# Performance work log

Hardware: AMD Instinct MI355X
Metric: run time of the kernel (lower is better)

The kernel has to match this reference:

```python
import jax, jax.numpy as jnp
import numpy as np

N, E, C, H, L = 20000, 200000, 64, 4, 2
L0_IN, E_IN, L0_OUT = 65, 15, 64
HC = H * C
EPS = 1e-5  # InstanceNorm1d default eps
NEG_SLOPE = 0.01  # F.leaky_relu default used by DGL EGATConv


def setup_inputs() -> dict:
    key = jax.random.key(0)
    ks = jax.random.split(key, 16)
    def s(k, shape, fan):
        return (jax.random.normal(k, shape, jnp.float32) / np.float32(np.sqrt(fan)))
    return {
        "x": jax.random.normal(ks[0], (N, L0_IN), jnp.float32),
        "efeat": jax.random.normal(ks[1], (E, E_IN), jnp.float32),
        "src": jax.random.randint(ks[2], (E,), 0, N, dtype=jnp.int32),
        "dst": jax.random.randint(ks[3], (E,), 0, N, dtype=jnp.int32),
        "Wn0": s(ks[4], (L0_IN, C), L0_IN),
        "bn0": jnp.zeros((C,), jnp.float32),
        "We0": s(ks[5], (E_IN, C), E_IN),
        "be0": jnp.zeros((C,), jnp.float32),
        "Wnode": s(ks[6], (L, C, HC), C),
        "bnode": jnp.zeros((L, HC), jnp.float32),
        "Wni": s(ks[7], (L, C, HC), C),
        "Wnj": s(ks[8], (L, C, HC), C),
        "Wfij": s(ks[9], (L, C, HC), C),
        "attn": s(ks[10], (L, H, C), C),
        "bias_e": jnp.zeros((L, HC), jnp.float32),
        "Wf": s(ks[11], (C, L0_OUT), C),
        "bf": jnp.zeros((L0_OUT,), jnp.float32),
    }


def _inorm(x):
    # InstanceNorm1d on a 2D [rows, channels] tensor == per-row normalization
    m = jnp.mean(x, axis=-1, keepdims=True)
    v = jnp.var(x, axis=-1, keepdims=True)
    return (x - m) * jax.lax.rsqrt(v + EPS)


def reference(x, efeat, src, dst, Wn0, bn0, We0, be0, Wnode, bnode,
              Wni, Wnj, Wfij, attn, bias_e, Wf, bf):
    h = x @ Wn0 + bn0        # [N, C]
    f = efeat @ We0 + be0    # [E, C]
    for l in range(L):
        # edge feature update: f_out = fc_ni(h)[src] + fc_nj(h)[dst] + fc_fij(f) + bias
        f_out = (h @ Wni[l])[src] + (h @ Wnj[l])[dst] + f @ Wfij[l] + bias_e[l]  # [E, HC]
        e = jax.nn.leaky_relu(f_out, NEG_SLOPE).reshape(E, H, C)
        score = jnp.einsum('ehc,hc->eh', e, attn[l])  # [E, H]
        # edge softmax over incoming edges of each destination node
        smax = jax.ops.segment_max(score, dst, num_segments=N)
        w = jnp.exp(score - smax[dst])
        denom = jax.ops.segment_sum(w, dst, num_segments=N)
        a = w / denom[dst]                                # [E, H]
        hproj = (h @ Wnode[l] + bnode[l]).reshape(N, H, C)
        msg = hproj[src] * a[:, :, None]                  # [E, H, C]
        h_new = jax.ops.segment_sum(msg, dst, num_segments=N)  # [N, H, C]
        # mean over heads -> InstanceNorm -> ELU
        h = jax.nn.elu(_inorm(jnp.mean(h_new, axis=1)))
        f = jax.nn.elu(_inorm(jnp.mean(f_out.reshape(E, H, C), axis=1)))
    return h @ Wf + bf
```

## Files before the change

kernel.cpp:

```cpp
#include <hip/hip_runtime.h>
#include <cmath>

#define NN 20000
#define NE 200000
#define SCAN_BLOCKS 79

typedef __attribute__((ext_vector_type(8))) short bf16x8;
typedef __attribute__((ext_vector_type(4))) float f32x4;
typedef unsigned int uint;

__device__ __forceinline__ float4 ld4(const float* p){ return *(const float4*)p; }

__device__ __forceinline__ uint packbf(float a, float b) {
  uint ua = __float_as_uint(a);
  uint ub = __float_as_uint(b);
  ua = (ua + 0x7fffu + ((ua >> 16) & 1u)) >> 16;
  ub = (ub + 0x7fffu + ((ub >> 16) & 1u)) >> 16;
  return ua | (ub << 16);
}
__device__ __forceinline__ float4 up4(uint2 u) {
  return make_float4(__uint_as_float(u.x << 16), __uint_as_float(u.x & 0xffff0000u),
                     __uint_as_float(u.y << 16), __uint_as_float(u.y & 0xffff0000u));
}

__global__ void gemm4_bf16(const float* __restrict__ A, const float* __restrict__ B,
                           const float* __restrict__ bias, uint2* __restrict__ O,
                           int M, int K, int Nout) {
  int jt = Nout >> 2;
  int idx = blockIdx.x * 256 + threadIdx.x;
  if (idx >= M * jt) return;
  int m = idx / jt;
  int j4 = (idx - m * jt) << 2;
  const float* a = A + (long)m * K;
  const float* b = B + j4;
  float ax = 0.f, ay = 0.f, az = 0.f, aw = 0.f;
  for (int k = 0; k < K; k++) {
    float av = a[k];
    float4 bv = ld4(b + (long)k * Nout);
    ax = fmaf(av, bv.x, ax); ay = fmaf(av, bv.y, ay);
    az = fmaf(av, bv.z, az); aw = fmaf(av, bv.w, aw);
  }
  if (bias) { float4 bb = ld4(bias + j4); ax += bb.x; ay += bb.y; az += bb.z; aw += bb.w; }
  O[(long)m * jt + (j4 >> 2)] = make_uint2(packbf(ax, ay), packbf(az, aw));
}

__global__ void zero_i32(int* __restrict__ p, int n) {
  int i = blockIdx.x * 256 + threadIdx.x;
  if (i < n) p[i] = 0;
}

__global__ void count_deg(const int* __restrict__ dst, int* __restrict__ deg) {
  int e = blockIdx.x * 256 + threadIdx.x;
  if (e < NE) atomicAdd(&deg[dst[e]], 1);
}

__global__ void scan1(const int* __restrict__ deg, int* __restrict__ off, int* __restrict__ bsum) {
  __shared__ int buf[256];
  int t = threadIdx.x;
  int g = blockIdx.x * 256 + t;
  int v = (g < NN) ? deg[g] : 0;
  buf[t] = v;
  __syncthreads();
  for (int s = 1; s < 256; s <<= 1) {
    int x = (t >= s) ? buf[t - s] : 0;
    __syncthreads();
    buf[t] += x;
    __syncthreads();
  }
  if (g < NN) off[g] = buf[t] - v;
  if (t == 255) bsum[blockIdx.x] = buf[255];
}

__global__ void scan2(int* __restrict__ bsum, int* __restrict__ off) {
  __shared__ int buf[128];
  int t = threadIdx.x;
  int v = (t < SCAN_BLOCKS) ? bsum[t] : 0;
  buf[t] = v;
  __syncthreads();
  for (int s = 1; s < 128; s <<= 1) {
    int x = (t >= s) ? buf[t - s] : 0;
    __syncthreads();
    buf[t] += x;
    __syncthreads();
  }
  if (t < SCAN_BLOCKS) bsum[t] = buf[t] - v;
  if (t == 127) off[NN] = buf[127];
}

__global__ void scan3(int* __restrict__ off, const int* __restrict__ bsum) {
  int g = blockIdx.x * 256 + threadIdx.x;
  if (g < NN) off[g] += bsum[blockIdx.x];
}

__global__ void fill_csr(const int* __restrict__ dst, const int* __restrict__ off,
                         int* __restrict__ cursor, int* __restrict__ elist) {
  int e = blockIdx.x * 256 + threadIdx.x;
  if (e >= NE) return;
  int d = dst[e];
  int p = atomicAdd(&cursor[d], 1);
  elist[off[d] + p] = e;
}

__global__ void prep_w(const float* __restrict__ Wni, const float* __restrict__ Wnj,
                       const float* __restrict__ Wfij, const float* __restrict__ Wnode,
                       uint* __restrict__ Wcat, uint* __restrict__ Wtn) {
  int rid = blockIdx.x * 256 + threadIdx.x;
  if (rid >= 1024) return;
  int l = rid >> 9, r = rid & 511;
  if (r < 256) {
    int c = r;
    uint* D = Wcat + (size_t)l * 24576 + c * 96;
    for (int k8 = 0; k8 < 24; k8++) {
      int ss = k8 >> 3;
      const float* S = (ss == 0 ? Wni : ss == 1 ? Wnj : Wfij) + l * 16384;
      int kl = (k8 & 7) * 8;
      uint u0 = packbf(S[(kl+0)*256 + c], S[(kl+1)*256 + c]);
      uint u1 = packbf(S[(kl+2)*256 + c], S[(kl+3)*256 + c]);
      uint u2 = packbf(S[(kl+4)*256 + c], S[(kl+5)*256 + c]);
      uint u3 = packbf(S[(kl+6)*256 + c], S[(kl+7)*256 + c]);
      *((uint4*)(D + k8 * 4)) = make_uint4(u0, u1, u2, u3);
    }
  } else {
    int c = r - 256;
    const float* S = Wnode + l * 16384;
    uint* D = Wtn + (size_t)l * 8192 + c * 32;
    for (int k8 = 0; k8 < 8; k8++) {
      int kl = k8 * 8;
      uint u0 = packbf(S[(kl+0)*256 + c], S[(kl+1)*256 + c]);
      uint u1 = packbf(S[(kl+2)*256 + c], S[(kl+3)*256 + c]);
      uint u2 = packbf(S[(kl+4)*256 + c], S[(kl+5)*256 + c]);
      uint u3 = packbf(S[(kl+6)*256 + c], S[(kl+7)*256 + c]);
      *((uint4*)(D + k8 * 4)) = make_uint4(u0, u1, u2, u3);
    }
  }
}

__global__ __launch_bounds__(256) void proj_mfma(
    const uint4* __restrict__ h_bf, const uint* __restrict__ Wtn_l,
    const float* __restrict__ bnd_l, uint2* __restrict__ hpj)
{
  int t = threadIdx.x, lane = t & 63, w = t >> 6;
  int col = lane & 15, quad = lane >> 4;
  bf16x8 A[4][2];
  #pragma unroll
  for (int tt = 0; tt < 4; tt++) {
    int c = (w * 4 + tt) * 16 + col;
    A[tt][0] = *(const bf16x8*)&Wtn_l[c * 32 + quad * 4];
    A[tt][1] = *(const bf16x8*)&Wtn_l[c * 32 + 16 + quad * 4];
  }
  for (int ch = 0; ch < 2; ch++) {
    int n = blockIdx.x * 32 + ch * 16 + col;
    bf16x8 b0 = *(const bf16x8*)&h_bf[(long)n * 8 + quad];
    bf16x8 b1 = *(const bf16x8*)&h_bf[(long)n * 8 + 4 + quad];
    #pragma unroll
    for (int tt = 0; tt < 4; tt++) {
      f32x4 acc = (f32x4){0.f, 0.f, 0.f, 0.f};
      acc = __builtin_amdgcn_mfma_f32_16x16x32_bf16(A[tt][0], b0, acc, 0, 0, 0);
      acc = __builtin_amdgcn_mfma_f32_16x16x32_bf16(A[tt][1], b1, acc, 0, 0, 0);
      int c = (w * 4 + tt) * 16 + quad * 4;
      float4 bb = ld4(bnd_l + c);
      hpj[(long)n * 64 + (c >> 2)] =
          make_uint2(packbf(acc[0] + bb.x, acc[1] + bb.y), packbf(acc[2] + bb.z, acc[3] + bb.w));
    }
  }
}

__global__ __launch_bounds__(256) void edge_mfma(
    const uint4* __restrict__ f_bf, const uint4* __restrict__ h_bf,
    const uint* __restrict__ Wcat_l, const float* __restrict__ be_l,
    const float* __restrict__ attn_l, const int* __restrict__ src,
    const int* __restrict__ dst, float* __restrict__ score,
    uint2* __restrict__ f_next)
{
  __shared__ float red[4][16][6];
  int t = threadIdx.x, lane = t & 63, w = t >> 6;
  int col = lane & 15, quad = lane >> 4;
  bf16x8 A[4][6];
  float4 be4[4], at4[4];
  #pragma unroll
  for (int hg = 0; hg < 4; hg++) {
    int c = (4 * hg + w) * 16 + col;
    #pragma unroll
    for (int kt = 0; kt < 6; kt++)
      A[hg][kt] = *(const bf16x8*)&Wcat_l[c * 96 + kt * 16 + quad * 4];
    int ce = (4 * hg + w) * 16 + quad * 4;
    be4[hg] = ld4(be_l + ce);
    at4[hg] = ld4(attn_l + ce);
  }
  #pragma unroll 1
  for (int ch = 0; ch < 8; ch++) {
    int e = blockIdx.x * 128 + ch * 16 + col;
    int ee = e < NE ? e : NE - 1;
    int s_ = src[ee], d_ = dst[ee];
    bf16x8 B[6];
    B[0] = *(const bf16x8*)&h_bf[(long)s_ * 8 + quad];
    B[1] = *(const bf16x8*)&h_bf[(long)s_ * 8 + 4 + quad];
    B[2] = *(const bf16x8*)&h_bf[(long)d_ * 8 + quad];
    B[3] = *(const bf16x8*)&h_bf[(long)d_ * 8 + 4 + quad];
    B[4] = *(const bf16x8*)&f_bf[(long)ee * 8 + quad];
    B[5] = *(const bf16x8*)&f_bf[(long)ee * 8 + 4 + quad];
    float m0 = 0.f, m1 = 0.f, m2 = 0.f, m3 = 0.f;
    float sh0 = 0.f, sh1 = 0.f, sh2 = 0.f, sh3 = 0.f;
    #pragma unroll
    for (int hg = 0; hg < 4; hg++) {
      f32x4 acc = (f32x4){0.f, 0.f, 0.f, 0.f};
      #pragma unroll
      for (int kt = 0; kt < 6; kt++)
        acc = __builtin_amdgcn_mfma_f32_16x16x32_bf16(A[hg][kt], B[kt], acc, 0, 0, 0);
      float x0 = acc[0] + be4[hg].x;
      float x1 = acc[1] + be4[hg].y;
      float x2 = acc[2] + be4[hg].z;
      float x3 = acc[3] + be4[hg].w;
      float l0 = x0 > 0.f ? x0 : 0.01f * x0;
      float l1 = x1 > 0.f ? x1 : 0.01f * x1;
      float l2 = x2 > 0.f ? x2 : 0.01f * x2;
      float l3 = x3 > 0.f ? x3 : 0.01f * x3;
      float dp = l0 * at4[hg].x + l1 * at4[hg].y + l2 * at4[hg].z + l3 * at4[hg].w;
      if (hg == 0) sh0 = dp; else if (hg == 1) sh1 = dp;
      else if (hg == 2) sh2 = dp; else sh3 = dp;
      m0 += x0; m1 += x1; m2 += x2; m3 += x3;
    }
    m0 *= 0.25f; m1 *= 0.25f; m2 *= 0.25f; m3 *= 0.25f;
    float s1 = m0 + m1 + m2 + m3;
    float s2 = m0 * m0 + m1 * m1 + m2 * m2 + m3 * m3;
    sh0 += __shfl_xor(sh0, 16); sh0 += __shfl_xor(sh0, 32);
    sh1 += __shfl_xor(sh1, 16); sh1 += __shfl_xor(sh1, 32);
    sh2 += __shfl_xor(sh2, 16); sh2 += __shfl_xor(sh2, 32);
    sh3 += __shfl_xor(sh3, 16); sh3 += __shfl_xor(sh3, 32);
    s1 += __shfl_xor(s1, 16); s1 += __shfl_xor(s1, 32);
    s2 += __shfl_xor(s2, 16); s2 += __shfl_xor(s2, 32);
    if (quad == 0) {
      red[w][col][0] = sh0; red[w][col][1] = sh1;
      red[w][col][2] = sh2; red[w][col][3] = sh3;
      red[w][col][4] = s1;  red[w][col][5] = s2;
    }
    __syncthreads();
    float svT = red[0][col][quad] + red[1][col][quad] + red[2][col][quad] + red[3][col][quad];
    float s1T = red[0][col][4] + red[1][col][4] + red[2][col][4] + red[3][col][4];
    float s2T = red[0][col][5] + red[1][col][5] + red[2][col][5] + red[3][col][5];
    __syncthreads();
    float mean = s1T * 0.015625f;
    float var  = s2T * 0.015625f - mean * mean;
    float rs = rsqrtf(var + 1e-5f);
    if (e < NE) {
      if (w == 0) score[e * 4 + quad] = svT;
      float o0 = (m0 - mean) * rs; o0 = o0 > 0.f ? o0 : expm1f(o0);
      float o1 = (m1 - mean) * rs; o1 = o1 > 0.f ? o1 : expm1f(o1);
      float o2 = (m2 - mean) * rs; o2 = o2 > 0.f ? o2 : expm1f(o2);
      float o3 = (m3 - mean) * rs; o3 = o3 > 0.f ? o3 : expm1f(o3);
      f_next[(long)e * 16 + w * 4 + quad] = make_uint2(packbf(o0, o1), packbf(o2, o3));
    }
  }
}

__global__ __launch_bounds__(256) void agg_kernel(
    const uint4* __restrict__ hproj, const float* __restrict__ score,
    const int* __restrict__ src, const int* __restrict__ elist,
    const int* __restrict__ off, uint4* __restrict__ h_next)
{
  int gw = (blockIdx.x * 256 + threadIdx.x) >> 6;
  int lane = threadIdx.x & 63;
  if (gw >= NN) return;
  int half = lane >> 5, seg = lane & 31;
  int hh = seg >> 3;
  int o0 = off[gw], o1 = off[gw + 1];
  if (o0 == o1) {
    if (lane < 8) h_next[(long)gw * 8 + lane] = make_uint4(0u, 0u, 0u, 0u);
    return;
  }
  float mx = -3.0e38f;
  for (int i = o0 + half; i < o1; i += 2)
    mx = fmaxf(mx, score[elist[i] * 4 + hh]);
  mx = fmaxf(mx, __shfl_xor(mx, 32));
  float a0 = 0.f, a1 = 0.f, a2 = 0.f, a3 = 0.f, a4 = 0.f, a5 = 0.f, a6 = 0.f, a7 = 0.f;
  float den = 0.f;
  for (int i = o0 + half; i < o1; i += 2) {
    int e = elist[i];
    float wgt = __expf(score[e * 4 + hh] - mx);
    den += wgt;
    uint4 v = hproj[(long)src[e] * 32 + seg];
    float4 p0 = up4(make_uint2(v.x, v.y));
    float4 p1 = up4(make_uint2(v.z, v.w));
    a0 = fmaf(wgt, p0.x, a0); a1 = fmaf(wgt, p0.y, a1);
    a2 = fmaf(wgt, p0.z, a2); a3 = fmaf(wgt, p0.w, a3);
    a4 = fmaf(wgt, p1.x, a4); a5 = fmaf(wgt, p1.y, a5);
    a6 = fmaf(wgt, p1.z, a6); a7 = fmaf(wgt, p1.w, a7);
  }
  den += __shfl_xor(den, 32);
  a0 += __shfl_xor(a0, 32); a1 += __shfl_xor(a1, 32);
  a2 += __shfl_xor(a2, 32); a3 += __shfl_xor(a3, 32);
  a4 += __shfl_xor(a4, 32); a5 += __shfl_xor(a5, 32);
  a6 += __shfl_xor(a6, 32); a7 += __shfl_xor(a7, 32);
  float inv = 1.f / den;
  float v0 = a0 * inv, v1 = a1 * inv, v2 = a2 * inv, v3 = a3 * inv;
  float v4 = a4 * inv, v5 = a5 * inv, v6 = a6 * inv, v7 = a7 * inv;
  v0 += __shfl_xor(v0, 8); v0 += __shfl_xor(v0, 16); v0 *= 0.25f;
  v1 += __shfl_xor(v1, 8); v1 += __shfl_xor(v1, 16); v1 *= 0.25f;
  v2 += __shfl_xor(v2, 8); v2 += __shfl_xor(v2, 16); v2 *= 0.25f;
  v3 += __shfl_xor(v3, 8); v3 += __shfl_xor(v3, 16); v3 *= 0.25f;
  v4 += __shfl_xor(v4, 8); v4 += __shfl_xor(v4, 16); v4 *= 0.25f;
  v5 += __shfl_xor(v5, 8); v5 += __shfl_xor(v5, 16); v5 *= 0.25f;
  v6 += __shfl_xor(v6, 8); v6 += __shfl_xor(v6, 16); v6 *= 0.25f;
  v7 += __shfl_xor(v7, 8); v7 += __shfl_xor(v7, 16); v7 *= 0.25f;
  float s1 = v0 + v1 + v2 + v3 + v4 + v5 + v6 + v7;
  float s2 = v0*v0 + v1*v1 + v2*v2 + v3*v3 + v4*v4 + v5*v5 + v6*v6 + v7*v7;
  s1 += __shfl_xor(s1, 1); s2 += __shfl_xor(s2, 1);
  s1 += __shfl_xor(s1, 2); s2 += __shfl_xor(s2, 2);
  s1 += __shfl_xor(s1, 4); s2 += __shfl_xor(s2, 4);
  float mean = s1 * 0.015625f;
  float var  = s2 * 0.015625f - mean * mean;
  float rs = rsqrtf(var + 1e-5f);
  if (lane < 8) {
    float o0 = (v0 - mean) * rs; o0 = o0 > 0.f ? o0 : expm1f(o0);
    float o1 = (v1 - mean) * rs; o1 = o1 > 0.f ? o1 : expm1f(o1);
    float o2 = (v2 - mean) * rs; o2 = o2 > 0.f ? o2 : expm1f(o2);
    float o3 = (v3 - mean) * rs; o3 = o3 > 0.f ? o3 : expm1f(o3);
    float o4 = (v4 - mean) * rs; o4 = o4 > 0.f ? o4 : expm1f(o4);
    float o5 = (v5 - mean) * rs; o5 = o5 > 0.f ? o5 : expm1f(o5);
    float o6 = (v6 - mean) * rs; o6 = o6 > 0.f ? o6 : expm1f(o6);
    float o7 = (v7 - mean) * rs; o7 = o7 > 0.f ? o7 : expm1f(o7);
    h_next[(long)gw * 8 + lane] =
        make_uint4(packbf(o0, o1), packbf(o2, o3), packbf(o4, o5), packbf(o6, o7));
  }
}

__global__ void final_gemm(const uint2* __restrict__ h, const float* __restrict__ Wf,
                           const float* __restrict__ bf_, float* __restrict__ out) {
  int idx = blockIdx.x * 256 + threadIdx.x;
  if (idx >= NN * 16) return;
  int m = idx >> 4, j4 = (idx & 15) << 2;
  const uint2* row = h + (long)m * 16;
  float ax = 0.f, ay = 0.f, az = 0.f, aw = 0.f;
  for (int kk = 0; kk < 16; kk++) {
    float4 a = up4(row[kk]);
    float4 b0 = ld4(Wf + (kk * 4 + 0) * 64 + j4);
    float4 b1 = ld4(Wf + (kk * 4 + 1) * 64 + j4);
    float4 b2 = ld4(Wf + (kk * 4 + 2) * 64 + j4);
    float4 b3 = ld4(Wf + (kk * 4 + 3) * 64 + j4);
    ax = fmaf(a.x, b0.x, ax); ay = fmaf(a.x, b0.y, ay); az = fmaf(a.x, b0.z, az); aw = fmaf(a.x, b0.w, aw);
    ax = fmaf(a.y, b1.x, ax); ay = fmaf(a.y, b1.y, ay); az = fmaf(a.y, b1.z, az); aw = fmaf(a.y, b1.w, aw);
    ax = fmaf(a.z, b2.x, ax); ay = fmaf(a.z, b2.y, ay); az = fmaf(a.z, b2.z, az); aw = fmaf(a.z, b2.w, aw);
    ax = fmaf(a.w, b3.x, ax); ay = fmaf(a.w, b3.y, ay); az = fmaf(a.w, b3.z, az); aw = fmaf(a.w, b3.w, aw);
  }
  float4 bb = ld4(bf_ + j4);
  *(float4*)(out + (long)m * 64 + j4) = make_float4(ax + bb.x, ay + bb.y, az + bb.z, aw + bb.w);
}

extern "C" void kernel_launch(void* const* d_in, const int* in_sizes, int n_in,
                              void* d_out, int out_size, void* d_ws, size_t ws_size,
                              hipStream_t stream) {
  const float* x      = (const float*)d_in[0];
  const float* efeat  = (const float*)d_in[1];
  const int*   src    = (const int*)d_in[2];
  const int*   dst    = (const int*)d_in[3];
  const float* Wn0    = (const float*)d_in[4];
  const float* bn0    = (const float*)d_in[5];
  const float* We0    = (const float*)d_in[6];
  const float* be0    = (const float*)d_in[7];
  const float* Wnode  = (const float*)d_in[8];
  const float* bnode  = (const float*)d_in[9];
  const float* Wni    = (const float*)d_in[10];
  const float* Wnj    = (const float*)d_in[11];
  const float* Wfij   = (const float*)d_in[12];
  const float* attn   = (const float*)d_in[13];
  const float* bias_e = (const float*)d_in[14];
  const float* Wf     = (const float*)d_in[15];
  const float* bf     = (const float*)d_in[16];
  float* out = (float*)d_out;

  char* w = (char*)d_ws;
  auto alloc = [&](size_t nbytes) { char* p = w; w += (nbytes + 255) & ~(size_t)255; return p; };
  uint2* h_a  = (uint2*)alloc((size_t)NN * 128);
  uint2* h_b  = (uint2*)alloc((size_t)NN * 128);
  uint2* f_a  = (uint2*)alloc((size_t)NE * 128);
  uint2* f_b  = (uint2*)alloc((size_t)NE * 128);
  uint2* hpj  = (uint2*)alloc((size_t)NN * 512);
  float* sc   = (float*)alloc((size_t)NE * 16);
  uint*  Wcat = (uint*)alloc((size_t)2 * 24576 * 4);
  uint*  Wtn  = (uint*)alloc((size_t)2 * 8192 * 4);
  int* deg    = (int*)alloc((size_t)NN * 2 * 4);
  int* cursor = deg + NN;
  int* off    = (int*)alloc((size_t)(NN + 1) * 4);
  int* elist  = (int*)alloc((size_t)NE * 4);
  int* bsum   = (int*)alloc((size_t)128 * 4);

  gemm4_bf16<<<(NN * 16 + 255) / 256, 256, 0, stream>>>(x, Wn0, bn0, h_a, NN, 65, 64);
  gemm4_bf16<<<(NE * 16 + 255) / 256, 256, 0, stream>>>(efeat, We0, be0, f_a, NE, 15, 64);
  prep_w<<<4, 256, 0, stream>>>(Wni, Wnj, Wfij, Wnode, Wcat, Wtn);

  zero_i32<<<(2 * NN + 255) / 256, 256, 0, stream>>>(deg, 2 * NN);
  count_deg<<<(NE + 255) / 256, 256, 0, stream>>>(dst, deg);
  scan1<<<SCAN_BLOCKS, 256, 0, stream>>>(deg, off, bsum);
  scan2<<<1, 128, 0, stream>>>(bsum, off);
  scan3<<<SCAN_BLOCKS, 256, 0, stream>>>(off, bsum);
  fill_csr<<<(NE + 255) / 256, 256, 0, stream>>>(dst, off, cursor, elist);

  uint2* hc = h_a; uint2* hn = h_b;
  uint2* fc = f_a; uint2* fn = f_b;
  for (int l = 0; l < 2; l++) {
    const uint* Wcat_l = Wcat + (size_t)l * 24576;
    const uint* Wtn_l  = Wtn + (size_t)l * 8192;
    const float* bnd_l = bnode + (size_t)l * 256;
    const float* be_l  = bias_e + (size_t)l * 256;
    const float* at_l  = attn + (size_t)l * 256;
    proj_mfma<<<625, 256, 0, stream>>>((const uint4*)hc, Wtn_l, bnd_l, hpj);
    edge_mfma<<<(NE + 127) / 128, 256, 0, stream>>>((const uint4*)fc, (const uint4*)hc,
                                                    Wcat_l, be_l, at_l, src, dst, sc, fn);
    agg_kernel<<<NN / 4, 256, 0, stream>>>((const uint4*)hpj, sc, src, elist, off,
                                           (uint4*)hn);
    uint2* tmp = hc; hc = hn; hn = tmp;
    tmp = fc; fc = fn; fn = tmp;
  }
  final_gemm<<<(NN * 16 + 255) / 256, 256, 0, stream>>>(hc, Wf, bf, out);
}
```

Measured before the change: 511.0 us.

## Aggregate raw h per head then project; split edge norm into fixup pass

```diff
diff --git a/kernel.cpp b/kernel.cpp
--- a/kernel.cpp
+++ b/kernel.cpp
@@ -92,23 +92,26 @@
   if (g < NN) off[g] += bsum[blockIdx.x];
 }
 
-__global__ void fill_csr(const int* __restrict__ dst, const int* __restrict__ off,
-                         int* __restrict__ cursor, int* __restrict__ elist) {
+__global__ void fill_csr(const int* __restrict__ dst, const int* __restrict__ src,
+                         const int* __restrict__ off, int* __restrict__ cursor,
+                         int* __restrict__ esrc, int* __restrict__ csr_pos) {
   int e = blockIdx.x * 256 + threadIdx.x;
   if (e >= NE) return;
   int d = dst[e];
   int p = atomicAdd(&cursor[d], 1);
-  elist[off[d] + p] = e;
+  int pos = off[d] + p;
+  esrc[pos] = src[e];
+  csr_pos[e] = pos;
 }
 
 __global__ void prep_w(const float* __restrict__ Wni, const float* __restrict__ Wnj,
                        const float* __restrict__ Wfij, const float* __restrict__ Wnode,
-                       uint* __restrict__ Wcat, uint* __restrict__ Wtn) {
+                       const float* __restrict__ bnode,
+                       uint* __restrict__ Wcat, uint* __restrict__ WcT,
+                       float* __restrict__ bmean) {
   int rid = blockIdx.x * 256 + threadIdx.x;
-  if (rid >= 1024) return;
-  int l = rid >> 9, r = rid & 511;
-  if (r < 256) {
-    int c = r;
+  if (rid < 512) {
+    int l = rid >> 8, c = rid & 255;
     uint* D = Wcat + (size_t)l * 24576 + c * 96;
     for (int k8 = 0; k8 < 24; k8++) {
       int ss = k8 >> 3;
@@ -120,48 +123,22 @@
       uint u3 = packbf(S[(kl+6)*256 + c], S[(kl+7)*256 + c]);
       *((uint4*)(D + k8 * 4)) = make_uint4(u0, u1, u2, u3);
     }
-  } else {
-    int c = r - 256;
+  } else if (rid < 640) {
+    int idx = rid - 512;
+    int l = idx >> 6, c = idx & 63;
     const float* S = Wnode + l * 16384;
-    uint* D = Wtn + (size_t)l * 8192 + c * 32;
-    for (int k8 = 0; k8 < 8; k8++) {
-      int kl = k8 * 8;
-      uint u0 = packbf(S[(kl+0)*256 + c], S[(kl+1)*256 + c]);
-      uint u1 = packbf(S[(kl+2)*256 + c], S[(kl+3)*256 + c]);
-      uint u2 = packbf(S[(kl+4)*256 + c], S[(kl+5)*256 + c]);
-      uint u3 = packbf(S[(kl+6)*256 + c], S[(kl+7)*256 + c]);
-      *((uint4*)(D + k8 * 4)) = make_uint4(u0, u1, u2, u3);
+    uint* D = WcT + (size_t)l * 8192 + c * 128;
+    for (int kp = 0; kp < 128; kp++) {
+      int k0 = kp * 2, k1 = kp * 2 + 1;
+      float v0 = S[(k0 & 63) * 256 + (k0 >> 6) * 64 + c] * 0.25f;
+      float v1 = S[(k1 & 63) * 256 + (k1 >> 6) * 64 + c] * 0.25f;
+      D[kp] = packbf(v0, v1);
     }
-  }
-}
-
-__global__ __launch_bounds__(256) void proj_mfma(
-    const uint4* __restrict__ h_bf, const uint* __restrict__ Wtn_l,
-    const float* __restrict__ bnd_l, uint2* __restrict__ hpj)
-{
-  int t = threadIdx.x, lane = t & 63, w = t >> 6;
-  int col = lane & 15, quad = lane >> 4;
-  bf16x8 A[4][2];
-  #pragma unroll
-  for (int tt = 0; tt < 4; tt++) {
-    int c = (w * 4 + tt) * 16 + col;
-    A[tt][0] = *(const bf16x8*)&Wtn_l[c * 32 + quad * 4];
-    A[tt][1] = *(const bf16x8*)&Wtn_l[c * 32 + 16 + quad * 4];
-  }
-  for (int ch = 0; ch < 2; ch++) {
-    int n = blockIdx.x * 32 + ch * 16 + col;
-    bf16x8 b0 = *(const bf16x8*)&h_bf[(long)n * 8 + quad];
-    bf16x8 b1 = *(const bf16x8*)&h_bf[(long)n * 8 + 4 + quad];
-    #pragma unroll
-    for (int tt = 0; tt < 4; tt++) {
-      f32x4 acc = (f32x4){0.f, 0.f, 0.f, 0.f};
-      acc = __builtin_amdgcn_mfma_f32_16x16x32_bf16(A[tt][0], b0, acc, 0, 0, 0);
-      acc = __builtin_amdgcn_mfma_f32_16x16x32_bf16(A[tt][1], b1, acc, 0, 0, 0);
-      int c = (w * 4 + tt) * 16 + quad * 4;
-      float4 bb = ld4(bnd_l + c);
-      hpj[(long)n * 64 + (c >> 2)] =
-          make_uint2(packbf(acc[0] + bb.x, acc[1] + bb.y), packbf(acc[2] + bb.z, acc[3] + bb.w));
-    }
+  } else if (rid < 768) {
+    int idx = rid - 640;
+    int l = idx >> 6, c = idx & 63;
+    const float* S = bnode + l * 256;
+    bmean[l * 64 + c] = 0.25f * (S[c] + S[64 + c] + S[128 + c] + S[192 + c]);
   }
 }
 
@@ -169,10 +146,9 @@
     const uint4* __restrict__ f_bf, const uint4* __restrict__ h_bf,
     const uint* __restrict__ Wcat_l, const float* __restrict__ be_l,
     const float* __restrict__ attn_l, const int* __restrict__ src,
-    const int* __restrict__ dst, float* __restrict__ score,
-    uint2* __restrict__ f_next)
+    const int* __restrict__ dst, float* __restrict__ sc_part,
+    uint2* __restrict__ f_mid)
 {
-  __shared__ float red[4][16][6];
   int t = threadIdx.x, lane = t & 63, w = t >> 6;
   int col = lane & 15, quad = lane >> 4;
   bf16x8 A[4][6];
@@ -188,17 +164,16 @@
     at4[hg] = ld4(attn_l + ce);
   }
   #pragma unroll 1
-  for (int ch = 0; ch < 8; ch++) {
-    int e = blockIdx.x * 128 + ch * 16 + col;
-    int ee = e < NE ? e : NE - 1;
-    int s_ = src[ee], d_ = dst[ee];
+  for (int ch = 0; ch < 4; ch++) {
+    int e = blockIdx.x * 64 + ch * 16 + col;
+    int s_ = src[e], d_ = dst[e];
     bf16x8 B[6];
     B[0] = *(const bf16x8*)&h_bf[(long)s_ * 8 + quad];
     B[1] = *(const bf16x8*)&h_bf[(long)s_ * 8 + 4 + quad];
     B[2] = *(const bf16x8*)&h_bf[(long)d_ * 8 + quad];
     B[3] = *(const bf16x8*)&h_bf[(long)d_ * 8 + 4 + quad];
-    B[4] = *(const bf16x8*)&f_bf[(long)ee * 8 + quad];
-    B[5] = *(const bf16x8*)&f_bf[(long)ee * 8 + 4 + quad];
+    B[4] = *(const bf16x8*)&f_bf[(long)e * 8 + quad];
+    B[5] = *(const bf16x8*)&f_bf[(long)e * 8 + 4 + quad];
     float m0 = 0.f, m1 = 0.f, m2 = 0.f, m3 = 0.f;
     float sh0 = 0.f, sh1 = 0.f, sh2 = 0.f, sh3 = 0.f;
     #pragma unroll
@@ -221,106 +196,156 @@
       m0 += x0; m1 += x1; m2 += x2; m3 += x3;
     }
     m0 *= 0.25f; m1 *= 0.25f; m2 *= 0.25f; m3 *= 0.25f;
-    float s1 = m0 + m1 + m2 + m3;
-    float s2 = m0 * m0 + m1 * m1 + m2 * m2 + m3 * m3;
     sh0 += __shfl_xor(sh0, 16); sh0 += __shfl_xor(sh0, 32);
     sh1 += __shfl_xor(sh1, 16); sh1 += __shfl_xor(sh1, 32);
     sh2 += __shfl_xor(sh2, 16); sh2 += __shfl_xor(sh2, 32);
     sh3 += __shfl_xor(sh3, 16); sh3 += __shfl_xor(sh3, 32);
-    s1 += __shfl_xor(s1, 16); s1 += __shfl_xor(s1, 32);
-    s2 += __shfl_xor(s2, 16); s2 += __shfl_xor(s2, 32);
-    if (quad == 0) {
-      red[w][col][0] = sh0; red[w][col][1] = sh1;
-      red[w][col][2] = sh2; red[w][col][3] = sh3;
-      red[w][col][4] = s1;  red[w][col][5] = s2;
-    }
-    __syncthreads();
-    float svT = red[0][col][quad] + red[1][col][quad] + red[2][col][quad] + red[3][col][quad];
-    float s1T = red[0][col][4] + red[1][col][4] + red[2][col][4] + red[3][col][4];
-    float s2T = red[0][col][5] + red[1][col][5] + red[2][col][5] + red[3][col][5];
-    __syncthreads();
-    float mean = s1T * 0.015625f;
-    float var  = s2T * 0.015625f - mean * mean;
-    float rs = rsqrtf(var + 1e-5f);
-    if (e < NE) {
-      if (w == 0) score[e * 4 + quad] = svT;
-      float o0 = (m0 - mean) * rs; o0 = o0 > 0.f ? o0 : expm1f(o0);
-      float o1 = (m1 - mean) * rs; o1 = o1 > 0.f ? o1 : expm1f(o1);
-      float o2 = (m2 - mean) * rs; o2 = o2 > 0.f ? o2 : expm1f(o2);
-      float o3 = (m3 - mean) * rs; o3 = o3 > 0.f ? o3 : expm1f(o3);
-      f_next[(long)e * 16 + w * 4 + quad] = make_uint2(packbf(o0, o1), packbf(o2, o3));
-    }
-  }
-}
-
-__global__ __launch_bounds__(256) void agg_kernel(
-    const uint4* __restrict__ hproj, const float* __restrict__ score,
-    const int* __restrict__ src, const int* __restrict__ elist,
-    const int* __restrict__ off, uint4* __restrict__ h_next)
+    if (quad == 0)
+      *(float4*)&sc_part[(long)e * 16 + w * 4] = make_float4(sh0, sh1, sh2, sh3);
+    f_mid[(long)e * 16 + w * 4 + quad] = make_uint2(packbf(m0, m1), packbf(m2, m3));
+  }
+}
+
+__global__ __launch_bounds__(256) void fixup(
+    const uint4* __restrict__ f_mid4, const float4* __restrict__ sc_part4,
+    const int* __restrict__ csr_pos, uint4* __restrict__ f_next4,
+    float4* __restrict__ sc_csr4)
 {
-  int gw = (blockIdx.x * 256 + threadIdx.x) >> 6;
-  int lane = threadIdx.x & 63;
-  if (gw >= NN) return;
-  int half = lane >> 5, seg = lane & 31;
-  int hh = seg >> 3;
-  int o0 = off[gw], o1 = off[gw + 1];
-  if (o0 == o1) {
-    if (lane < 8) h_next[(long)gw * 8 + lane] = make_uint4(0u, 0u, 0u, 0u);
-    return;
-  }
-  float mx = -3.0e38f;
-  for (int i = o0 + half; i < o1; i += 2)
-    mx = fmaxf(mx, score[elist[i] * 4 + hh]);
-  mx = fmaxf(mx, __shfl_xor(mx, 32));
-  float a0 = 0.f, a1 = 0.f, a2 = 0.f, a3 = 0.f, a4 = 0.f, a5 = 0.f, a6 = 0.f, a7 = 0.f;
-  float den = 0.f;
-  for (int i = o0 + half; i < o1; i += 2) {
-    int e = elist[i];
-    float wgt = __expf(score[e * 4 + hh] - mx);
-    den += wgt;
-    uint4 v = hproj[(long)src[e] * 32 + seg];
-    float4 p0 = up4(make_uint2(v.x, v.y));
-    float4 p1 = up4(make_uint2(v.z, v.w));
-    a0 = fmaf(wgt, p0.x, a0); a1 = fmaf(wgt, p0.y, a1);
-    a2 = fmaf(wgt, p0.z, a2); a3 = fmaf(wgt, p0.w, a3);
-    a4 = fmaf(wgt, p1.x, a4); a5 = fmaf(wgt, p1.y, a5);
-    a6 = fmaf(wgt, p1.z, a6); a7 = fmaf(wgt, p1.w, a7);
-  }
-  den += __shfl_xor(den, 32);
-  a0 += __shfl_xor(a0, 32); a1 += __shfl_xor(a1, 32);
-  a2 += __shfl_xor(a2, 32); a3 += __shfl_xor(a3, 32);
-  a4 += __shfl_xor(a4, 32); a5 += __shfl_xor(a5, 32);
-  a6 += __shfl_xor(a6, 32); a7 += __shfl_xor(a7, 32);
-  float inv = 1.f / den;
-  float v0 = a0 * inv, v1 = a1 * inv, v2 = a2 * inv, v3 = a3 * inv;
-  float v4 = a4 * inv, v5 = a5 * inv, v6 = a6 * inv, v7 = a7 * inv;
-  v0 += __shfl_xor(v0, 8); v0 += __shfl_xor(v0, 16); v0 *= 0.25f;
-  v1 += __shfl_xor(v1, 8); v1 += __shfl_xor(v1, 16); v1 *= 0.25f;
-  v2 += __shfl_xor(v2, 8); v2 += __shfl_xor(v2, 16); v2 *= 0.25f;
-  v3 += __shfl_xor(v3, 8); v3 += __shfl_xor(v3, 16); v3 *= 0.25f;
-  v4 += __shfl_xor(v4, 8); v4 += __shfl_xor(v4, 16); v4 *= 0.25f;
-  v5 += __shfl_xor(v5, 8); v5 += __shfl_xor(v5, 16); v5 *= 0.25f;
-  v6 += __shfl_xor(v6, 8); v6 += __shfl_xor(v6, 16); v6 *= 0.25f;
-  v7 += __shfl_xor(v7, 8); v7 += __shfl_xor(v7, 16); v7 *= 0.25f;
-  float s1 = v0 + v1 + v2 + v3 + v4 + v5 + v6 + v7;
-  float s2 = v0*v0 + v1*v1 + v2*v2 + v3*v3 + v4*v4 + v5*v5 + v6*v6 + v7*v7;
+  int tid = blockIdx.x * 256 + threadIdx.x;
+  int e = tid >> 3, sub = tid & 7;
+  uint4 mv = f_mid4[(long)e * 8 + sub];
+  float4 p0 = up4(make_uint2(mv.x, mv.y));
+  float4 p1 = up4(make_uint2(mv.z, mv.w));
+  float s1 = p0.x + p0.y + p0.z + p0.w + p1.x + p1.y + p1.z + p1.w;
+  float s2 = p0.x*p0.x + p0.y*p0.y + p0.z*p0.z + p0.w*p0.w
+           + p1.x*p1.x + p1.y*p1.y + p1.z*p1.z + p1.w*p1.w;
   s1 += __shfl_xor(s1, 1); s2 += __shfl_xor(s2, 1);
   s1 += __shfl_xor(s1, 2); s2 += __shfl_xor(s2, 2);
   s1 += __shfl_xor(s1, 4); s2 += __shfl_xor(s2, 4);
   float mean = s1 * 0.015625f;
   float var  = s2 * 0.015625f - mean * mean;
   float rs = rsqrtf(var + 1e-5f);
-  if (lane < 8) {
-    float o0 = (v0 - mean) * rs; o0 = o0 > 0.f ? o0 : expm1f(o0);
-    float o1 = (v1 - mean) * rs; o1 = o1 > 0.f ? o1 : expm1f(o1);
-    float o2 = (v2 - mean) * rs; o2 = o2 > 0.f ? o2 : expm1f(o2);
-    float o3 = (v3 - mean) * rs; o3 = o3 > 0.f ? o3 : expm1f(o3);
-    float o4 = (v4 - mean) * rs; o4 = o4 > 0.f ? o4 : expm1f(o4);
-    float o5 = (v5 - mean) * rs; o5 = o5 > 0.f ? o5 : expm1f(o5);
-    float o6 = (v6 - mean) * rs; o6 = o6 > 0.f ? o6 : expm1f(o6);
-    float o7 = (v7 - mean) * rs; o7 = o7 > 0.f ? o7 : expm1f(o7);
-    h_next[(long)gw * 8 + lane] =
-        make_uint4(packbf(o0, o1), packbf(o2, o3), packbf(o4, o5), packbf(o6, o7));
+  float o0 = (p0.x - mean) * rs; o0 = o0 > 0.f ? o0 : expm1f(o0);
+  float o1 = (p0.y - mean) * rs; o1 = o1 > 0.f ? o1 : expm1f(o1);
+  float o2 = (p0.z - mean) * rs; o2 = o2 > 0.f ? o2 : expm1f(o2);
+  float o3 = (p0.w - mean) * rs; o3 = o3 > 0.f ? o3 : expm1f(o3);
+  float o4 = (p1.x - mean) * rs; o4 = o4 > 0.f ? o4 : expm1f(o4);
+  float o5 = (p1.y - mean) * rs; o5 = o5 > 0.f ? o5 : expm1f(o5);
+  float o6 = (p1.z - mean) * rs; o6 = o6 > 0.f ? o6 : expm1f(o6);
+  float o7 = (p1.w - mean) * rs; o7 = o7 > 0.f ? o7 : expm1f(o7);
+  f_next4[(long)e * 8 + sub] =
+      make_uint4(packbf(o0, o1), packbf(o2, o3), packbf(o4, o5), packbf(o6, o7));
+  if (sub < 4) {
+    float4 sp = sc_part4[(long)e * 4 + sub];
+    sp.x += __shfl_xor(sp.x, 1); sp.y += __shfl_xor(sp.y, 1);
+    sp.z += __shfl_xor(sp.z, 1); sp.w += __shfl_xor(sp.w, 1);
+    sp.x += __shfl_xor(sp.x, 2); sp.y += __shfl_xor(sp.y, 2);
+    sp.z += __shfl_xor(sp.z, 2); sp.w += __shfl_xor(sp.w, 2);
+    if (sub == 0) sc_csr4[csr_pos[e]] = sp;
+  }
+}
+
+__global__ __launch_bounds__(256) void agg_kernel(
+    const uint* __restrict__ h_u, const float4* __restrict__ sc_csr4,
+    const int* __restrict__ esrc, const int* __restrict__ off,
+    uint* __restrict__ g_u)
+{
+  int n = (blockIdx.x * 256 + threadIdx.x) >> 6;
+  int lane = threadIdx.x & 63;
+  int half = lane >> 5, seg = lane & 31;
+  int o0 = off[n], o1 = off[n + 1];
+  if (o0 == o1) {
+    g_u[(long)n * 128 + (half * 2) * 32 + seg] = 0u;
+    g_u[(long)n * 128 + (half * 2 + 1) * 32 + seg] = 0u;
+    return;
+  }
+  float mx0 = -3.0e38f, mx1 = -3.0e38f, mx2 = -3.0e38f, mx3 = -3.0e38f;
+  for (int i = o0 + half; i < o1; i += 2) {
+    float4 s = sc_csr4[i];
+    mx0 = fmaxf(mx0, s.x); mx1 = fmaxf(mx1, s.y);
+    mx2 = fmaxf(mx2, s.z); mx3 = fmaxf(mx3, s.w);
+  }
+  mx0 = fmaxf(mx0, __shfl_xor(mx0, 32)); mx1 = fmaxf(mx1, __shfl_xor(mx1, 32));
+  mx2 = fmaxf(mx2, __shfl_xor(mx2, 32)); mx3 = fmaxf(mx3, __shfl_xor(mx3, 32));
+  float d0 = 0.f, d1 = 0.f, d2 = 0.f, d3 = 0.f;
+  float a00=0.f,a01=0.f,a10=0.f,a11=0.f,a20=0.f,a21=0.f,a30=0.f,a31=0.f;
+  for (int i = o0 + half; i < o1; i += 2) {
+    float4 s = sc_csr4[i];
+    float w0 = __expf(s.x - mx0), w1 = __expf(s.y - mx1);
+    float w2 = __expf(s.z - mx2), w3 = __expf(s.w - mx3);
+    d0 += w0; d1 += w1; d2 += w2; d3 += w3;
+    int sr = esrc[i];
+    uint hv = h_u[(long)sr * 32 + seg];
+    float hlo = __uint_as_float(hv << 16);
+    float hhi = __uint_as_float(hv & 0xffff0000u);
+    a00 = fmaf(w0, hlo, a00); a01 = fmaf(w0, hhi, a01);
+    a10 = fmaf(w1, hlo, a10); a11 = fmaf(w1, hhi, a11);
+    a20 = fmaf(w2, hlo, a20); a21 = fmaf(w2, hhi, a21);
+    a30 = fmaf(w3, hlo, a30); a31 = fmaf(w3, hhi, a31);
+  }
+  d0 += __shfl_xor(d0, 32); d1 += __shfl_xor(d1, 32);
+  d2 += __shfl_xor(d2, 32); d3 += __shfl_xor(d3, 32);
+  a00 += __shfl_xor(a00, 32); a01 += __shfl_xor(a01, 32);
+  a10 += __shfl_xor(a10, 32); a11 += __shfl_xor(a11, 32);
+  a20 += __shfl_xor(a20, 32); a21 += __shfl_xor(a21, 32);
+  a30 += __shfl_xor(a30, 32); a31 += __shfl_xor(a31, 32);
+  float i0 = 1.f / d0, i1 = 1.f / d1, i2 = 1.f / d2, i3 = 1.f / d3;
+  uint u0 = packbf(a00 * i0, a01 * i0);
+  uint u1 = packbf(a10 * i1, a11 * i1);
+  uint u2 = packbf(a20 * i2, a21 * i2);
+  uint u3 = packbf(a30 * i3, a31 * i3);
+  if (half == 0) {
+    g_u[(long)n * 128 + seg] = u0;
+    g_u[(long)n * 128 + 32 + seg] = u1;
+  } else {
+    g_u[(long)n * 128 + 64 + seg] = u2;
+    g_u[(long)n * 128 + 96 + seg] = u3;
+  }
+}
+
+__global__ __launch_bounds__(256) void combine(
+    const uint4* __restrict__ g4, const uint4* __restrict__ WcT4,
+    const float* __restrict__ bmean_l, const int* __restrict__ off,
+    uint2* __restrict__ h_next)
+{
+  __shared__ float red[2][4][16][2];
+  int t = threadIdx.x, lane = t & 63, w = t >> 6;
+  int col = lane & 15, quad = lane >> 4;
+  int c = w * 16 + col;
+  bf16x8 A[8];
+  #pragma unroll
+  for (int kt = 0; kt < 8; kt++)
+    A[kt] = *(const bf16x8*)&WcT4[c * 32 + kt * 4 + quad];
+  int c2 = w * 16 + quad * 4;
+  float4 bm = ld4(bmean_l + c2);
+  for (int ch = 0; ch < 2; ch++) {
+    int n = blockIdx.x * 32 + ch * 16 + col;
+    int deg = off[n + 1] - off[n];
+    f32x4 acc = (f32x4){0.f, 0.f, 0.f, 0.f};
+    #pragma unroll
+    for (int kt = 0; kt < 8; kt++) {
+      bf16x8 B = *(const bf16x8*)&g4[(long)n * 32 + kt * 4 + quad];
+      acc = __builtin_amdgcn_mfma_f32_16x16x32_bf16(A[kt], B, acc, 0, 0, 0);
+    }
+    float x0, x1, x2, x3;
+    if (deg > 0) { x0 = acc[0] + bm.x; x1 = acc[1] + bm.y; x2 = acc[2] + bm.z; x3 = acc[3] + bm.w; }
+    else { x0 = x1 = x2 = x3 = 0.f; }
+    float s1 = x0 + x1 + x2 + x3;
+    float s2 = x0*x0 + x1*x1 + x2*x2 + x3*x3;
+    s1 += __shfl_xor(s1, 16); s2 += __shfl_xor(s2, 16);
+    s1 += __shfl_xor(s1, 32); s2 += __shfl_xor(s2, 32);
+    if (quad == 0) { red[ch][w][col][0] = s1; red[ch][w][col][1] = s2; }
+    __syncthreads();
+    float s1T = red[ch][0][col][0] + red[ch][1][col][0] + red[ch][2][col][0] + red[ch][3][col][0];
+    float s2T = red[ch][0][col][1] + red[ch][1][col][1] + red[ch][2][col][1] + red[ch][3][col][1];
+    float mean = s1T * 0.015625f;
+    float var  = s2T * 0.015625f - mean * mean;
+    float rs = rsqrtf(var + 1e-5f);
+    float o0 = (x0 - mean) * rs; o0 = o0 > 0.f ? o0 : expm1f(o0);
+    float o1 = (x1 - mean) * rs; o1 = o1 > 0.f ? o1 : expm1f(o1);
+    float o2 = (x2 - mean) * rs; o2 = o2 > 0.f ? o2 : expm1f(o2);
+    float o3 = (x3 - mean) * rs; o3 = o3 > 0.f ? o3 : expm1f(o3);
+    h_next[(long)n * 16 + w * 4 + quad] = make_uint2(packbf(o0, o1), packbf(o2, o3));
   }
 }
 
@@ -370,44 +395,50 @@
 
   char* w = (char*)d_ws;
   auto alloc = [&](size_t nbytes) { char* p = w; w += (nbytes + 255) & ~(size_t)255; return p; };
-  uint2* h_a  = (uint2*)alloc((size_t)NN * 128);
-  uint2* h_b  = (uint2*)alloc((size_t)NN * 128);
-  uint2* f_a  = (uint2*)alloc((size_t)NE * 128);
-  uint2* f_b  = (uint2*)alloc((size_t)NE * 128);
-  uint2* hpj  = (uint2*)alloc((size_t)NN * 512);
-  float* sc   = (float*)alloc((size_t)NE * 16);
-  uint*  Wcat = (uint*)alloc((size_t)2 * 24576 * 4);
-  uint*  Wtn  = (uint*)alloc((size_t)2 * 8192 * 4);
-  int* deg    = (int*)alloc((size_t)NN * 2 * 4);
-  int* cursor = deg + NN;
-  int* off    = (int*)alloc((size_t)(NN + 1) * 4);
-  int* elist  = (int*)alloc((size_t)NE * 4);
-  int* bsum   = (int*)alloc((size_t)128 * 4);
+  uint2* h_a   = (uint2*)alloc((size_t)NN * 128);
+  uint2* h_b   = (uint2*)alloc((size_t)NN * 128);
+  uint2* f_a   = (uint2*)alloc((size_t)NE * 128);
+  uint2* f_b   = (uint2*)alloc((size_t)NE * 128);
+  uint2* f_mid = (uint2*)alloc((size_t)NE * 128);
+  float* scp   = (float*)alloc((size_t)NE * 64);
+  float* scc   = (float*)alloc((size_t)NE * 16);
+  uint*  g     = (uint*)alloc((size_t)NN * 512);
+  uint*  Wcat  = (uint*)alloc((size_t)2 * 24576 * 4);
+  uint*  WcT   = (uint*)alloc((size_t)2 * 8192 * 4);
+  float* bmean = (float*)alloc((size_t)2 * 64 * 4);
+  int* deg     = (int*)alloc((size_t)NN * 2 * 4);
+  int* cursor  = deg + NN;
+  int* off     = (int*)alloc((size_t)(NN + 1) * 4);
+  int* esrc    = (int*)alloc((size_t)NE * 4);
+  int* csr_pos = (int*)alloc((size_t)NE * 4);
+  int* bsum    = (int*)alloc((size_t)128 * 4);
 
   gemm4_bf16<<<(NN * 16 + 255) / 256, 256, 0, stream>>>(x, Wn0, bn0, h_a, NN, 65, 64);
   gemm4_bf16<<<(NE * 16 + 255) / 256, 256, 0, stream>>>(efeat, We0, be0, f_a, NE, 15, 64);
-  prep_w<<<4, 256, 0, stream>>>(Wni, Wnj, Wfij, Wnode, Wcat, Wtn);
+  prep_w<<<4, 256, 0, stream>>>(Wni, Wnj, Wfij, Wnode, bnode, Wcat, WcT, bmean);
 
   zero_i32<<<(2 * NN + 255) / 256, 256, 0, stream>>>(deg, 2 * NN);
   count_deg<<<(NE + 255) / 256, 256, 0, stream>>>(dst, deg);
   scan1<<<SCAN_BLOCKS, 256, 0, stream>>>(deg, off, bsum);
   scan2<<<1, 128, 0, stream>>>(bsum, off);
   scan3<<<SCAN_BLOCKS, 256, 0, stream>>>(off, bsum);
-  fill_csr<<<(NE + 255) / 256, 256, 0, stream>>>(dst, off, cursor, elist);
+  fill_csr<<<(NE + 255) / 256, 256, 0, stream>>>(dst, src, off, cursor, esrc, csr_pos);
 
   uint2* hc = h_a; uint2* hn = h_b;
   uint2* fc = f_a; uint2* fn = f_b;
   for (int l = 0; l < 2; l++) {
     const uint* Wcat_l = Wcat + (size_t)l * 24576;
-    const uint* Wtn_l  = Wtn + (size_t)l * 8192;
-    const float* bnd_l = bnode + (size_t)l * 256;
+    const uint4* WcT_l = (const uint4*)(WcT + (size_t)l * 8192);
+    const float* bm_l  = bmean + (size_t)l * 64;
     const float* be_l  = bias_e + (size_t)l * 256;
     const float* at_l  = attn + (size_t)l * 256;
-    proj_mfma<<<625, 256, 0, stream>>>((const uint4*)hc, Wtn_l, bnd_l, hpj);
-    edge_mfma<<<(NE + 127) / 128, 256, 0, stream>>>((const uint4*)fc, (const uint4*)hc,
-                                                    Wcat_l, be_l, at_l, src, dst, sc, fn);
-    agg_kernel<<<NN / 4, 256, 0, stream>>>((const uint4*)hpj, sc, src, elist, off,
-                                           (uint4*)hn);
+    edge_mfma<<<NE / 64, 256, 0, stream>>>((const uint4*)fc, (const uint4*)hc,
+                                           Wcat_l, be_l, at_l, src, dst, scp, f_mid);
+    fixup<<<NE / 32, 256, 0, stream>>>((const uint4*)f_mid, (const float4*)scp,
+                                       csr_pos, (uint4*)fn, (float4*)scc);
+    agg_kernel<<<NN / 4, 256, 0, stream>>>((const uint*)hc, (const float4*)scc,
+                                           esrc, off, g);
+    combine<<<NN / 32, 256, 0, stream>>>((const uint4*)g, WcT_l, bm_l, off, hn);
     uint2* tmp = hc; hc = hn; hn = tmp;
     tmp = fc; fc = fn; fn = tmp;
   }
```

Result: faster. 500.2 us (-2.1%).
